# Optimization experiments

Hardware: AMD Instinct MI355X
Metric: run time of the kernel (lower is better)

## Reference

```python
import jax, jax.numpy as jnp
import numpy as np

N_NODES = 50000
N_EDGES = 1600000
IN_CH = 128
HID = 32
HEADS = 2
OUT_CH = 128
N_GRAPHS = 64
NEG_SLOPE = 0.2


def setup_inputs() -> dict:
    key = jax.random.key(0)
    ks = jax.random.split(key, 12)
    x = jax.random.normal(ks[0], (N_NODES, IN_CH), dtype=jnp.float32)
    edge_index = jax.random.randint(ks[1], (2, N_EDGES), 0, N_NODES, dtype=jnp.int64)
    batch = jnp.sort(jax.random.randint(ks[2], (N_NODES,), 0, N_GRAPHS, dtype=jnp.int64))
    s = 0.1
    return {
        "x": x,
        "edge_index": edge_index,
        "batch": batch,
        # conv1: GATConv(IN_CH, 32, heads=2), concat=True -> out 64
        "W1": jax.random.normal(ks[3], (IN_CH, HEADS * HID), dtype=jnp.float32) * s,
        "att_src1": jax.random.normal(ks[4], (HEADS, HID), dtype=jnp.float32) * s,
        "att_dst1": jax.random.normal(ks[5], (HEADS, HID), dtype=jnp.float32) * s,
        "b1": jnp.zeros((HEADS * HID,), dtype=jnp.float32),
        # conv2: GATConv(64, OUT_CH, heads=1)
        "W2": jax.random.normal(ks[6], (HEADS * HID, OUT_CH), dtype=jnp.float32) * s,
        "att_src2": jax.random.normal(ks[7], (1, OUT_CH), dtype=jnp.float32) * s,
        "att_dst2": jax.random.normal(ks[8], (1, OUT_CH), dtype=jnp.float32) * s,
        "b2": jnp.zeros((OUT_CH,), dtype=jnp.float32),
    }


def gat_conv(x, src, dst, W, att_src, att_dst, bias, heads, out_dim):
    """PyG GATConv: edges src->dst, softmax over incoming edges per dst node."""
    n = x.shape[0]
    xl = (x @ W).reshape(n, heads, out_dim)                 # [N,H,D]
    a_s = jnp.sum(xl * att_src, axis=-1)                    # [N,H]
    a_d = jnp.sum(xl * att_dst, axis=-1)                    # [N,H]
    e = jax.nn.leaky_relu(a_s[src] + a_d[dst], NEG_SLOPE)   # [E,H]
    e_max = jax.lax.stop_gradient(jax.ops.segment_max(e, dst, num_segments=n))
    ex = jnp.exp(e - e_max[dst])
    denom = jax.ops.segment_sum(ex, dst, num_segments=n)
    alpha = ex / denom[dst]                                 # [E,H]
    msg = xl[src] * alpha[:, :, None]                       # [E,H,D]
    out = jax.ops.segment_sum(msg, dst, num_segments=n)     # [N,H,D]
    return out.reshape(n, heads * out_dim) + bias


def reference(x, edge_index, batch, W1, att_src1, att_dst1, b1, W2, att_src2, att_dst2, b2):
    n = x.shape[0]
    loop = jnp.arange(n, dtype=edge_index.dtype)
    src = jnp.concatenate([edge_index[0], loop])  # add_self_loops (PyG default)
    dst = jnp.concatenate([edge_index[1], loop])
    h = gat_conv(x, src, dst, W1, att_src1, att_dst1, b1, HEADS, HID)
    h = jax.nn.elu(h)
    h = gat_conv(h, src, dst, W2, att_src2, att_dst2, b2, 1, OUT_CH)
    h = jax.nn.elu(h)
    # global_mean_pool
    sums = jax.ops.segment_sum(h, batch, num_segments=N_GRAPHS)
    cnts = jax.ops.segment_sum(jnp.ones((n,), dtype=h.dtype), batch, num_segments=N_GRAPHS)
    return sums / jnp.maximum(cnts, 1.0)[:, None]
```

## Files before the change

### kernel.cpp

```cpp
#include <hip/hip_runtime.h>

#define N_NODES 50000
#define N_EDGES 1600000
#define E_TOT   (N_EDGES + N_NODES)
#define IN_CH   128
#define C1      64
#define OUT_CH  128
#define N_GRAPHS 64
#define NEG_SLOPE 0.2f

#define BSH   7
#define NBUCK ((N_NODES + 127) / 128)
#define BCAP  5120
#define CHUNK 8192
#define PN    32

typedef __attribute__((ext_vector_type(8))) short bf16x8;
typedef __attribute__((ext_vector_type(4))) float f32x4;

__device__ __forceinline__ float elu_f(float v) {
    return v > 0.f ? v : (__expf(v) - 1.f);
}
__device__ __forceinline__ unsigned short f2bf(float f) {
    unsigned u = __float_as_uint(f);
    return (unsigned short)((u + 0x7FFFu + ((u >> 16) & 1u)) >> 16);
}
__device__ __forceinline__ float bf_lo(unsigned u) { return __uint_as_float(u << 16); }
__device__ __forceinline__ float bf_hi(unsigned u) { return __uint_as_float(u & 0xFFFF0000u); }

__global__ __launch_bounds__(256) void k_gemm1(
    const float* __restrict__ x, const float* __restrict__ W1,
    const float* __restrict__ att_s, const float* __restrict__ att_d,
    unsigned short* __restrict__ xl1, float* __restrict__ a_s, float* __restrict__ a_d)
{
    __shared__ unsigned short W1T[64][136];
    __shared__ float psA[4][16], psD[4][16];
    const int t = threadIdx.x, wave = t >> 6, lane = t & 63;
    const int quad = lane >> 4, lm = lane & 15;
    for (int i = t; i < 128 * 64; i += 256)
        W1T[i & 63][i >> 6] = f2bf(W1[i]);
    __syncthreads();

    const int n0 = wave * 16;
    const int c  = n0 + lm;
    bf16x8 bfr[4];
    #pragma unroll
    for (int s = 0; s < 4; ++s)
        bfr[s] = *(const bf16x8*)&W1T[c][s * 32 + quad * 8];
    const float asc = att_s[c], adc = att_d[c];

    const int r0 = blockIdx.x * 16;
    f32x4 acc = {0.f, 0.f, 0.f, 0.f};
    #pragma unroll
    for (int s = 0; s < 4; ++s) {
        const float* xp = &x[(size_t)(r0 + lm) * 128 + s * 32 + quad * 8];
        float4 xa = *(const float4*)xp;
        float4 xb = *(const float4*)(xp + 4);
        bf16x8 afr;
        afr[0] = (short)f2bf(xa.x); afr[1] = (short)f2bf(xa.y);
        afr[2] = (short)f2bf(xa.z); afr[3] = (short)f2bf(xa.w);
        afr[4] = (short)f2bf(xb.x); afr[5] = (short)f2bf(xb.y);
        afr[6] = (short)f2bf(xb.z); afr[7] = (short)f2bf(xb.w);
        acc = __builtin_amdgcn_mfma_f32_16x16x32_bf16(afr, bfr[s], acc, 0, 0, 0);
    }
    float psv[4], pdv[4];
    #pragma unroll
    for (int r = 0; r < 4; ++r) {
        float v = acc[r];
        xl1[(size_t)(r0 + quad * 4 + r) * 64 + c] = f2bf(v);
        psv[r] = v * asc;
        pdv[r] = v * adc;
    }
    #pragma unroll
    for (int ofs = 1; ofs <= 8; ofs <<= 1) {
        #pragma unroll
        for (int r = 0; r < 4; ++r) {
            psv[r] += __shfl_xor(psv[r], ofs, 64);
            pdv[r] += __shfl_xor(pdv[r], ofs, 64);
        }
    }
    if (lm == 0) {
        #pragma unroll
        for (int r = 0; r < 4; ++r) {
            psA[wave][quad * 4 + r] = psv[r];
            psD[wave][quad * 4 + r] = pdv[r];
        }
    }
    __syncthreads();
    if (t < 32) {
        const int row = t & 15, h = t >> 4;
        a_s[(size_t)(r0 + row) * 2 + h] = psA[2 * h][row] + psA[2 * h + 1][row];
        a_d[(size_t)(r0 + row) * 2 + h] = psD[2 * h][row] + psD[2 * h + 1][row];
    }
}

__global__ __launch_bounds__(256) void k_bin(
    const int* __restrict__ ei, int* __restrict__ gcur, unsigned* __restrict__ bbuf)
{
    __shared__ int cnt[512];
    __shared__ int base[NBUCK];
    __shared__ int cnt2[NBUCK];
    __shared__ int gpos[NBUCK];
    __shared__ unsigned stage[CHUNK];
    __shared__ unsigned short bof[CHUNK];
    const int t = threadIdx.x;
    const long long e0 = (long long)blockIdx.x * CHUNK;
    const int nE = (int)min((long long)CHUNK, (long long)E_TOT - e0);

    cnt[t] = 0; cnt[t + 256] = 0;
    for (int b = t; b < NBUCK; b += 256) cnt2[b] = 0;
    __syncthreads();

    const int per = CHUNK / 256;
    int myb[per]; unsigned mye[per];
    #pragma unroll
    for (int i = 0; i < per; ++i) {
        int idx = t + 256 * i;
        myb[i] = -1;
        if (idx < nE) {
            long long e = e0 + idx;
            int s, d;
            if (e < N_EDGES) { s = ei[e]; d = ei[N_EDGES + e]; }
            else             { s = d = (int)(e - N_EDGES); }
            myb[i] = d >> BSH;
            mye[i] = ((unsigned)(d & 127) << 17) | (unsigned)s;
            atomicAdd(&cnt[myb[i]], 1);
        }
    }
    __syncthreads();
    for (int ofs = 1; ofs < 512; ofs <<= 1) {
        int v0 = (t >= ofs) ? cnt[t - ofs] : 0;
        int v1 = cnt[t + 256 - ofs];
        __syncthreads();
        cnt[t] += v0; cnt[t + 256] += v1;
        __syncthreads();
    }
    for (int b = t; b < NBUCK; b += 256) {
        base[b] = (b == 0) ? 0 : cnt[b - 1];
        int c = cnt[b] - base[b];
        gpos[b] = (c > 0) ? atomicAdd(&gcur[b], c) : 0;
    }
    __syncthreads();
    #pragma unroll
    for (int i = 0; i < per; ++i) {
        if (myb[i] >= 0) {
            int slot = base[myb[i]] + atomicAdd(&cnt2[myb[i]], 1);
            stage[slot] = mye[i];
            bof[slot] = (unsigned short)myb[i];
        }
    }
    __syncthreads();
    for (int i = t; i < nE; i += 256) {
        int b = bof[i];
        int pos = gpos[b] + (i - base[b]);
        if (pos < BCAP)
            bbuf[(size_t)b * BCAP + pos] = stage[i];
    }
}

__global__ __launch_bounds__(256) void k_bsort(
    const int* __restrict__ gcur, unsigned* __restrict__ bbuf,
    int* __restrict__ beg, int* __restrict__ end)
{
    __shared__ unsigned est[BCAP];
    __shared__ unsigned sst[BCAP];
    __shared__ int c[128], lbase[128], c2[128];
    const int b = blockIdx.x, t = threadIdx.x;
    const int n = min(gcur[b], BCAP);
    unsigned* reg = bbuf + (size_t)b * BCAP;
    for (int i = t; i < n; i += 256) est[i] = reg[i];
    if (t < 128) { c[t] = 0; c2[t] = 0; }
    __syncthreads();
    for (int i = t; i < n; i += 256) atomicAdd(&c[est[i] >> 17], 1);
    __syncthreads();
    for (int ofs = 1; ofs < 128; ofs <<= 1) {
        int v = (t < 128 && t >= ofs) ? c[t - ofs] : 0;
        __syncthreads();
        if (t < 128) c[t] += v;
        __syncthreads();
    }
    if (t < 128) {
        lbase[t] = (t == 0) ? 0 : c[t - 1];
        int dst = (b << BSH) + t;
        if (dst < N_NODES) {
            beg[dst] = b * BCAP + lbase[t];
            end[dst] = b * BCAP + c[t];
        }
    }
    __syncthreads();
    for (int i = t; i < n; i += 256) {
        unsigned v = est[i];
        int dl = (int)(v >> 17);
        int pos = lbase[dl] + atomicAdd(&c2[dl], 1);
        sst[pos] = v & 0x1FFFFu;
    }
    __syncthreads();
    for (int i = t; i < n; i += 256) reg[i] = sst[i];
}

__global__ __launch_bounds__(256) void k_attn1g2(
    const int* __restrict__ beg_a, const int* __restrict__ end_a,
    const unsigned* __restrict__ csr,
    const float* __restrict__ a_s, const float* __restrict__ a_d,
    const unsigned short* __restrict__ xl,
    const float* __restrict__ b1, const float* __restrict__ W2,
    const float* __restrict__ att_s2, const float* __restrict__ att_d2,
    unsigned* __restrict__ xl2p,
    float* __restrict__ a_s2, float* __restrict__ a_d2)
{
    __shared__ unsigned W2p[C1 * 64];
    __shared__ float hbuf[4][C1];
    const int t = threadIdx.x, wave = t >> 6, lane = t & 63;
    for (int i = t; i < C1 * 64; i += 256) {
        int k = i >> 6, p = i & 63;
        unsigned lo = f2bf(W2[k * 128 + 2 * p]);
        unsigned hi = f2bf(W2[k * 128 + 2 * p + 1]);
        W2p[i] = lo | (hi << 16);
    }
    const int dst = blockIdx.x * 4 + wave;
    const int beg = beg_a[dst], end = end_a[dst];
    const float ad0 = a_d[dst * 2], ad1 = a_d[dst * 2 + 1];
    const int li = lane & 7, sub = lane >> 3;
    const float4 b1a = *(const float4*)&b1[li * 8];
    const float4 b1b = *(const float4*)&b1[li * 8 + 4];
    const float2 as2c = *(const float2*)&att_s2[2 * lane];
    const float2 ad2c = *(const float2*)&att_d2[2 * lane];
    __syncthreads();

    float acc[8];
    #pragma unroll
    for (int i = 0; i < 8; ++i) acc[i] = 0.f;
    float ws0 = 0.f, ws1 = 0.f;
    for (int base = beg; base < end; base += 64) {
        const int cnt = min(64, end - base);
        int s = 0; float w0 = 0.f, w1 = 0.f;
        if (base + lane < end) {
            s = (int)csr[base + lane];
            float e0 = a_s[s * 2] + ad0;     e0 = e0 > 0.f ? e0 : NEG_SLOPE * e0;
            float e1 = a_s[s * 2 + 1] + ad1; e1 = e1 > 0.f ? e1 : NEG_SLOPE * e1;
            w0 = __expf(e0);
            w1 = __expf(e1);
        }
        ws0 += w0; ws1 += w1;
        for (int k = 0; k < cnt; k += 32) {
            {
                const int ia = k + sub;
                int   sa  = __shfl(s, ia, 64);
                float wa0 = __shfl(w0, ia, 64);
                float wa1 = __shfl(w1, ia, 64);
                float wa = (li < 4) ? wa0 : wa1;
                uint4 va = *(const uint4*)&xl[(size_t)sa * 64 + li * 8];
                acc[0] = fmaf(bf_lo(va.x), wa, acc[0]); acc[1] = fmaf(bf_hi(va.x), wa, acc[1]);
                acc[2] = fmaf(bf_lo(va.y), wa, acc[2]); acc[3] = fmaf(bf_hi(va.y), wa, acc[3]);
                acc[4] = fmaf(bf_lo(va.z), wa, acc[4]); acc[5] = fmaf(bf_hi(va.z), wa, acc[5]);
                acc[6] = fmaf(bf_lo(va.w), wa, acc[6]); acc[7] = fmaf(bf_hi(va.w), wa, acc[7]);
            }
            if (k + 8 < cnt) {
                const int ib = k + 8 + sub;
                int   sb  = __shfl(s, ib, 64);
                float wb0 = __shfl(w0, ib, 64);
                float wb1 = __shfl(w1, ib, 64);
                float wb = (li < 4) ? wb0 : wb1;
                uint4 vb = *(const uint4*)&xl[(size_t)sb * 64 + li * 8];
                acc[0] = fmaf(bf_lo(vb.x), wb, acc[0]); acc[1] = fmaf(bf_hi(vb.x), wb, acc[1]);
                acc[2] = fmaf(bf_lo(vb.y), wb, acc[2]); acc[3] = fmaf(bf_hi(vb.y), wb, acc[3]);
                acc[4] = fmaf(bf_lo(vb.z), wb, acc[4]); acc[5] = fmaf(bf_hi(vb.z), wb, acc[5]);
                acc[6] = fmaf(bf_lo(vb.w), wb, acc[6]); acc[7] = fmaf(bf_hi(vb.w), wb, acc[7]);
            }
            if (k + 16 < cnt) {
                const int ic = k + 16 + sub;
                int   sc  = __shfl(s, ic, 64);
                float wc0 = __shfl(w0, ic, 64);
                float wc1 = __shfl(w1, ic, 64);
                float wc = (li < 4) ? wc0 : wc1;
                uint4 vc = *(const uint4*)&xl[(size_t)sc * 64 + li * 8];
                acc[0] = fmaf(bf_lo(vc.x), wc, acc[0]); acc[1] = fmaf(bf_hi(vc.x), wc, acc[1]);
                acc[2] = fmaf(bf_lo(vc.y), wc, acc[2]); acc[3] = fmaf(bf_hi(vc.y), wc, acc[3]);
                acc[4] = fmaf(bf_lo(vc.z), wc, acc[4]); acc[5] = fmaf(bf_hi(vc.z), wc, acc[5]);
                acc[6] = fmaf(bf_lo(vc.w), wc, acc[6]); acc[7] = fmaf(bf_hi(vc.w), wc, acc[7]);
            }
            if (k + 24 < cnt) {
                const int id = k + 24 + sub;
                int   sd  = __shfl(s, id, 64);
                float wd0 = __shfl(w0, id, 64);
                float wd1 = __shfl(w1, id, 64);
                float wd = (li < 4) ? wd0 : wd1;
                uint4 vd = *(const uint4*)&xl[(size_t)sd * 64 + li * 8];
                acc[0] = fmaf(bf_lo(vd.x), wd, acc[0]); acc[1] = fmaf(bf_hi(vd.x), wd, acc[1]);
                acc[2] = fmaf(bf_lo(vd.y), wd, acc[2]); acc[3] = fmaf(bf_hi(vd.y), wd, acc[3]);
                acc[4] = fmaf(bf_lo(vd.z), wd, acc[4]); acc[5] = fmaf(bf_hi(vd.z), wd, acc[5]);
                acc[6] = fmaf(bf_lo(vd.w), wd, acc[6]); acc[7] = fmaf(bf_hi(vd.w), wd, acc[7]);
            }
        }
    }
    #pragma unroll
    for (int ofs = 32; ofs >= 1; ofs >>= 1) {
        ws0 += __shfl_xor(ws0, ofs, 64);
        ws1 += __shfl_xor(ws1, ofs, 64);
    }
    #pragma unroll
    for (int ofs = 8; ofs <= 32; ofs <<= 1) {
        #pragma unroll
        for (int i = 0; i < 8; ++i) acc[i] += __shfl_xor(acc[i], ofs, 64);
    }
    {
        const float inv = 1.f / ((li < 4) ? ws0 : ws1);
        float h0 = elu_f(acc[0] * inv + b1a.x);
        float h1 = elu_f(acc[1] * inv + b1a.y);
        float h2 = elu_f(acc[2] * inv + b1a.z);
        float h3 = elu_f(acc[3] * inv + b1a.w);
        float h4 = elu_f(acc[4] * inv + b1b.x);
        float h5 = elu_f(acc[5] * inv + b1b.y);
        float h6 = elu_f(acc[6] * inv + b1b.z);
        float h7 = elu_f(acc[7] * inv + b1b.w);
        if (sub == 0) {
            float4 p0; p0.x = h0; p0.y = h1; p0.z = h2; p0.w = h3;
            float4 p1; p1.x = h4; p1.y = h5; p1.z = h6; p1.w = h7;
            *(float4*)&hbuf[wave][li * 8]     = p0;
            *(float4*)&hbuf[wave][li * 8 + 4] = p1;
        }
    }
    __syncthreads();

    float o0 = 0.f, o1 = 0.f;
    #pragma unroll
    for (int k = 0; k < C1; k += 2) {
        float2 hk = *(const float2*)&hbuf[wave][k];
        unsigned p0 = W2p[k * 64 + lane];
        unsigned p1 = W2p[(k + 1) * 64 + lane];
        o0 = fmaf(bf_lo(p0), hk.x, o0); o1 = fmaf(bf_hi(p0), hk.x, o1);
        o0 = fmaf(bf_lo(p1), hk.y, o0); o1 = fmaf(bf_hi(p1), hk.y, o1);
    }
    float ps = o0 * as2c.x + o1 * as2c.y;
    float pd = o0 * ad2c.x + o1 * ad2c.y;
    #pragma unroll
    for (int ofs = 32; ofs >= 1; ofs >>= 1) {
        ps += __shfl_xor(ps, ofs, 64);
        pd += __shfl_xor(pd, ofs, 64);
    }
    if (lane == 0) { a_s2[dst] = ps; a_d2[dst] = pd; }
    unsigned pk = (unsigned)f2bf(o0) | ((unsigned)f2bf(o1) << 16);
    xl2p[(size_t)dst * 64 + lane] = pk;
}

__global__ __launch_bounds__(256) void k_attn2(
    const int* __restrict__ beg_a, const int* __restrict__ end_a,
    const unsigned* __restrict__ csr,
    const float* __restrict__ a_s, const float* __restrict__ a_d,
    const unsigned short* __restrict__ xl, float* __restrict__ out)
{
    const int wave = threadIdx.x >> 6, lane = threadIdx.x & 63;
    const int dst = blockIdx.x * 4 + wave;
    const int beg = beg_a[dst], end = end_a[dst];
    const float ad0 = a_d[dst];

    const int li = lane & 15, sub = lane >> 4;
    float acc[8];
    #pragma unroll
    for (int i = 0; i < 8; ++i) acc[i] = 0.f;
    float ws0 = 0.f;
    for (int base = beg; base < end; base += 64) {
        const int cnt = min(64, end - base);
        int s = 0; float w0 = 0.f;
        if (base + lane < end) {
            s = (int)csr[base + lane];
            float e0 = a_s[s] + ad0; e0 = e0 > 0.f ? e0 : NEG_SLOPE * e0;
            w0 = __expf(e0);
        }
        ws0 += w0;
        for (int k = 0; k < cnt; k += 16) {
            {
                const int ia = k + sub;
                int   sa = __shfl(s, ia, 64);
                float wa = __shfl(w0, ia, 64);
                uint4 va = *(const uint4*)&xl[(size_t)sa * 128 + li * 8];
                acc[0] = fmaf(bf_lo(va.x), wa, acc[0]); acc[1] = fmaf(bf_hi(va.x), wa, acc[1]);
                acc[2] = fmaf(bf_lo(va.y), wa, acc[2]); acc[3] = fmaf(bf_hi(va.y), wa, acc[3]);
                acc[4] = fmaf(bf_lo(va.z), wa, acc[4]); acc[5] = fmaf(bf_hi(va.z), wa, acc[5]);
                acc[6] = fmaf(bf_lo(va.w), wa, acc[6]); acc[7] = fmaf(bf_hi(va.w), wa, acc[7]);
            }
            if (k + 4 < cnt) {
                const int ib = k + 4 + sub;
                int   sb = __shfl(s, ib, 64);
                float wb = __shfl(w0, ib, 64);
                uint4 vb = *(const uint4*)&xl[(size_t)sb * 128 + li * 8];
                acc[0] = fmaf(bf_lo(vb.x), wb, acc[0]); acc[1] = fmaf(bf_hi(vb.x), wb, acc[1]);
                acc[2] = fmaf(bf_lo(vb.y), wb, acc[2]); acc[3] = fmaf(bf_hi(vb.y), wb, acc[3]);
                acc[4] = fmaf(bf_lo(vb.z), wb, acc[4]); acc[5] = fmaf(bf_hi(vb.z), wb, acc[5]);
                acc[6] = fmaf(bf_lo(vb.w), wb, acc[6]); acc[7] = fmaf(bf_hi(vb.w), wb, acc[7]);
            }
            if (k + 8 < cnt) {
                const int ic = k + 8 + sub;
                int   sc = __shfl(s, ic, 64);
                float wc = __shfl(w0, ic, 64);
                uint4 vc = *(const uint4*)&xl[(size_t)sc * 128 + li * 8];
                acc[0] = fmaf(bf_lo(vc.x), wc, acc[0]); acc[1] = fmaf(bf_hi(vc.x), wc, acc[1]);
                acc[2] = fmaf(bf_lo(vc.y), wc, acc[2]); acc[3] = fmaf(bf_hi(vc.y), wc, acc[3]);
                acc[4] = fmaf(bf_lo(vc.z), wc, acc[4]); acc[5] = fmaf(bf_hi(vc.z), wc, acc[5]);
                acc[6] = fmaf(bf_lo(vc.w), wc, acc[6]); acc[7] = fmaf(bf_hi(vc.w), wc, acc[7]);
            }
            if (k + 12 < cnt) {
                const int id = k + 12 + sub;
                int   sd = __shfl(s, id, 64);
                float wd = __shfl(w0, id, 64);
                uint4 vd = *(const uint4*)&xl[(size_t)sd * 128 + li * 8];
                acc[0] = fmaf(bf_lo(vd.x), wd, acc[0]); acc[1] = fmaf(bf_hi(vd.x), wd, acc[1]);
                acc[2] = fmaf(bf_lo(vd.y), wd, acc[2]); acc[3] = fmaf(bf_hi(vd.y), wd, acc[3]);
                acc[4] = fmaf(bf_lo(vd.z), wd, acc[4]); acc[5] = fmaf(bf_hi(vd.z), wd, acc[5]);
                acc[6] = fmaf(bf_lo(vd.w), wd, acc[6]); acc[7] = fmaf(bf_hi(vd.w), wd, acc[7]);
            }
        }
    }
    #pragma unroll
    for (int ofs = 32; ofs >= 1; ofs >>= 1)
        ws0 += __shfl_xor(ws0, ofs, 64);
    #pragma unroll
    for (int ofs = 16; ofs <= 32; ofs <<= 1) {
        #pragma unroll
        for (int i = 0; i < 8; ++i) acc[i] += __shfl_xor(acc[i], ofs, 64);
    }
    if (lane < 16) {
        const float inv = 1.f / ws0;
        float4 r0, r1;
        r0.x = acc[0]*inv; r0.y = acc[1]*inv; r0.z = acc[2]*inv; r0.w = acc[3]*inv;
        r1.x = acc[4]*inv; r1.y = acc[5]*inv; r1.z = acc[6]*inv; r1.w = acc[7]*inv;
        *(float4*)&out[(size_t)dst * 128 + li * 8]     = r0;
        *(float4*)&out[(size_t)dst * 128 + li * 8 + 4] = r1;
    }
}

__global__ __launch_bounds__(256) void k_pool(
    const float* __restrict__ out2, const float* __restrict__ b2,
    const int* __restrict__ batch, float* __restrict__ sums, float* __restrict__ cnts)
{
    const int c    = threadIdx.x & 127;
    const int half = threadIdx.x >> 7;
    const int n0   = blockIdx.x * PN;
    const int nb   = n0 + half;
    if (nb >= N_NODES) return;
    const float bc = b2[c];
    float acc = 0.f;
    int cur = batch[nb], cnt = 0;
    for (int i = half; i < PN; i += 2) {
        int n = n0 + i;
        if (n >= N_NODES) break;
        int g = batch[n];
        if (g != cur) {
            atomicAdd(&sums[cur * OUT_CH + c], acc);
            if (c == 0) atomicAdd(&cnts[cur], (float)cnt);
            acc = 0.f; cnt = 0; cur = g;
        }
        acc += elu_f(out2[(size_t)n * OUT_CH + c] + bc);
        cnt++;
    }
    if (cnt > 0) {
        atomicAdd(&sums[cur * OUT_CH + c], acc);
        if (c == 0) atomicAdd(&cnts[cur], (float)cnt);
    }
}

__global__ __launch_bounds__(256) void k_final(
    const float* __restrict__ sums, const float* __restrict__ cnts,
    float* __restrict__ out)
{
    int i = blockIdx.x * 256 + threadIdx.x;
    if (i >= N_GRAPHS * OUT_CH) return;
    out[i] = sums[i] / fmaxf(cnts[i >> 7], 1.f);
}

extern "C" void kernel_launch(void* const* d_in, const int* in_sizes, int n_in,
                              void* d_out, int out_size, void* d_ws, size_t ws_size,
                              hipStream_t stream)
{
    const float* x    = (const float*)d_in[0];
    const int*   ei   = (const int*)d_in[1];
    const int*   batch= (const int*)d_in[2];
    const float* W1   = (const float*)d_in[3];
    const float* as1  = (const float*)d_in[4];
    const float* ad1  = (const float*)d_in[5];
    const float* b1   = (const float*)d_in[6];
    const float* W2   = (const float*)d_in[7];
    const float* as2  = (const float*)d_in[8];
    const float* ad2  = (const float*)d_in[9];
    const float* b2   = (const float*)d_in[10];

    float* ws = (float*)d_ws;
    size_t o = 0;
    unsigned short* xl1b = (unsigned short*)(ws + o); o += (size_t)N_NODES * C1 / 2;
    unsigned*       xl2p = (unsigned*)(ws + o);       o += (size_t)N_NODES * 64;
    float*    a_s1 = ws + o; o += (size_t)N_NODES * 2;
    float*    a_d1 = ws + o; o += (size_t)N_NODES * 2;
    float*    a_s2 = ws + o; o += (size_t)N_NODES;
    float*    a_d2 = ws + o; o += (size_t)N_NODES;
    float*    out2 = ws + o; o += (size_t)N_NODES * OUT_CH;
    unsigned* bbuf = (unsigned*)(ws + o); o += (size_t)NBUCK * BCAP;
    int*      beg  = (int*)(ws + o); o += (size_t)N_NODES;
    int*      end  = (int*)(ws + o); o += (size_t)N_NODES;
    size_t zero_start = o;
    int*      gcur = (int*)(ws + o); o += (size_t)NBUCK;
    float*    sums = ws + o;         o += (size_t)N_GRAPHS * OUT_CH;
    float*    cnts = ws + o;         o += (size_t)N_GRAPHS;
    size_t zero_bytes = (o - zero_start) * sizeof(float);
    hipMemsetAsync(ws + zero_start, 0, zero_bytes, stream);

    const int nchunks = (E_TOT + CHUNK - 1) / CHUNK;
    k_bin<<<nchunks, 256, 0, stream>>>(ei, gcur, bbuf);
    k_bsort<<<NBUCK, 256, 0, stream>>>(gcur, bbuf, beg, end);

    k_gemm1<<<N_NODES / 16, 256, 0, stream>>>(x, W1, as1, ad1, xl1b, a_s1, a_d1);
    k_attn1g2<<<N_NODES / 4, 256, 0, stream>>>(beg, end, bbuf, a_s1, a_d1, xl1b,
                                               b1, W2, as2, ad2, xl2p, a_s2, a_d2);
    k_attn2<<<N_NODES / 4, 256, 0, stream>>>(beg, end, bbuf, a_s2, a_d2,
                                             (const unsigned short*)xl2p, out2);
    k_pool<<<(N_NODES + PN - 1) / PN, 256, 0, stream>>>(out2, b2, batch, sums, cnts);
    k_final<<<(N_GRAPHS * OUT_CH + 255) / 256, 256, 0, stream>>>(sums, cnts, (float*)d_out);
}
```

Baseline: 298.9 us.

## Split layer-2 projection out of attention kernel into separate MFMA GEMM

The second-layer linear projection, previously fused per destination node into the layer-1 attention kernel as scalar FMAs from shared memory, now runs in its own kernel using bf16 MFMA 16x16x32 instructions over 16-row tiles. The layer-1 attention kernel now only writes the ELU-activated hidden features in bf16 to a new buffer. This removes the per-block W2 staging into LDS and the extra __syncthreads from the attention kernel, which may raise its occupancy and cut its instruction count. The cost is an extra kernel launch and a global-memory round trip of the hidden activations, plus an additional bf16 rounding of the hidden features.

New measurement: 282.3 us. -5.6%, faster.

```diff
diff --git a/kernel.cpp b/kernel.cpp
--- a/kernel.cpp
+++ b/kernel.cpp
@@ -198,34 +198,21 @@
     for (int i = t; i < n; i += 256) reg[i] = sst[i];
 }
 
-__global__ __launch_bounds__(256) void k_attn1g2(
+__global__ __launch_bounds__(256) void k_attn1(
     const int* __restrict__ beg_a, const int* __restrict__ end_a,
     const unsigned* __restrict__ csr,
     const float* __restrict__ a_s, const float* __restrict__ a_d,
     const unsigned short* __restrict__ xl,
-    const float* __restrict__ b1, const float* __restrict__ W2,
-    const float* __restrict__ att_s2, const float* __restrict__ att_d2,
-    unsigned* __restrict__ xl2p,
-    float* __restrict__ a_s2, float* __restrict__ a_d2)
-{
-    __shared__ unsigned W2p[C1 * 64];
-    __shared__ float hbuf[4][C1];
-    const int t = threadIdx.x, wave = t >> 6, lane = t & 63;
-    for (int i = t; i < C1 * 64; i += 256) {
-        int k = i >> 6, p = i & 63;
-        unsigned lo = f2bf(W2[k * 128 + 2 * p]);
-        unsigned hi = f2bf(W2[k * 128 + 2 * p + 1]);
-        W2p[i] = lo | (hi << 16);
-    }
+    const float* __restrict__ b1,
+    unsigned short* __restrict__ hout)
+{
+    const int wave = threadIdx.x >> 6, lane = threadIdx.x & 63;
     const int dst = blockIdx.x * 4 + wave;
     const int beg = beg_a[dst], end = end_a[dst];
     const float ad0 = a_d[dst * 2], ad1 = a_d[dst * 2 + 1];
     const int li = lane & 7, sub = lane >> 3;
     const float4 b1a = *(const float4*)&b1[li * 8];
     const float4 b1b = *(const float4*)&b1[li * 8 + 4];
-    const float2 as2c = *(const float2*)&att_s2[2 * lane];
-    const float2 ad2c = *(const float2*)&att_d2[2 * lane];
-    __syncthreads();
 
     float acc[8];
     #pragma unroll
@@ -303,7 +290,7 @@
         #pragma unroll
         for (int i = 0; i < 8; ++i) acc[i] += __shfl_xor(acc[i], ofs, 64);
     }
-    {
+    if (sub == 0) {
         const float inv = 1.f / ((li < 4) ? ws0 : ws1);
         float h0 = elu_f(acc[0] * inv + b1a.x);
         float h1 = elu_f(acc[1] * inv + b1a.y);
@@ -313,34 +300,77 @@
         float h5 = elu_f(acc[5] * inv + b1b.y);
         float h6 = elu_f(acc[6] * inv + b1b.z);
         float h7 = elu_f(acc[7] * inv + b1b.w);
-        if (sub == 0) {
-            float4 p0; p0.x = h0; p0.y = h1; p0.z = h2; p0.w = h3;
-            float4 p1; p1.x = h4; p1.y = h5; p1.z = h6; p1.w = h7;
-            *(float4*)&hbuf[wave][li * 8]     = p0;
-            *(float4*)&hbuf[wave][li * 8 + 4] = p1;
-        }
-    }
-    __syncthreads();
-
-    float o0 = 0.f, o1 = 0.f;
-    #pragma unroll
-    for (int k = 0; k < C1; k += 2) {
-        float2 hk = *(const float2*)&hbuf[wave][k];
-        unsigned p0 = W2p[k * 64 + lane];
-        unsigned p1 = W2p[(k + 1) * 64 + lane];
-        o0 = fmaf(bf_lo(p0), hk.x, o0); o1 = fmaf(bf_hi(p0), hk.x, o1);
-        o0 = fmaf(bf_lo(p1), hk.y, o0); o1 = fmaf(bf_hi(p1), hk.y, o1);
-    }
-    float ps = o0 * as2c.x + o1 * as2c.y;
-    float pd = o0 * ad2c.x + o1 * ad2c.y;
-    #pragma unroll
-    for (int ofs = 32; ofs >= 1; ofs >>= 1) {
-        ps += __shfl_xor(ps, ofs, 64);
-        pd += __shfl_xor(pd, ofs, 64);
-    }
-    if (lane == 0) { a_s2[dst] = ps; a_d2[dst] = pd; }
-    unsigned pk = (unsigned)f2bf(o0) | ((unsigned)f2bf(o1) << 16);
-    xl2p[(size_t)dst * 64 + lane] = pk;
+        uint4 p;
+        p.x = (unsigned)f2bf(h0) | ((unsigned)f2bf(h1) << 16);
+        p.y = (unsigned)f2bf(h2) | ((unsigned)f2bf(h3) << 16);
+        p.z = (unsigned)f2bf(h4) | ((unsigned)f2bf(h5) << 16);
+        p.w = (unsigned)f2bf(h6) | ((unsigned)f2bf(h7) << 16);
+        *(uint4*)&hout[(size_t)dst * 64 + li * 8] = p;
+    }
+}
+
+__global__ __launch_bounds__(256) void k_gemm2m(
+    const unsigned short* __restrict__ h, const float* __restrict__ W2,
+    const float* __restrict__ att_s, const float* __restrict__ att_d,
+    unsigned short* __restrict__ xl2, float* __restrict__ a_s, float* __restrict__ a_d)
+{
+    __shared__ unsigned short W2T[128][72];
+    __shared__ float psA[4][16], psD[4][16];
+    const int t = threadIdx.x, wave = t >> 6, lane = t & 63;
+    const int quad = lane >> 4, lm = lane & 15;
+    for (int i = t; i < 64 * 128; i += 256)
+        W2T[i & 127][i >> 7] = f2bf(W2[i]);
+    __syncthreads();
+
+    const int c0 = wave * 32 + lm;
+    const int c1 = c0 + 16;
+    bf16x8 bfr0[2], bfr1[2];
+    #pragma unroll
+    for (int s = 0; s < 2; ++s) {
+        bfr0[s] = *(const bf16x8*)&W2T[c0][s * 32 + quad * 8];
+        bfr1[s] = *(const bf16x8*)&W2T[c1][s * 32 + quad * 8];
+    }
+    const float as0 = att_s[c0], as1 = att_s[c1];
+    const float ad0 = att_d[c0], ad1 = att_d[c1];
+
+    const int r0 = blockIdx.x * 16;
+    f32x4 acc0 = {0.f, 0.f, 0.f, 0.f}, acc1 = {0.f, 0.f, 0.f, 0.f};
+    #pragma unroll
+    for (int s = 0; s < 2; ++s) {
+        bf16x8 afr = *(const bf16x8*)&h[(size_t)(r0 + lm) * 64 + s * 32 + quad * 8];
+        acc0 = __builtin_amdgcn_mfma_f32_16x16x32_bf16(afr, bfr0[s], acc0, 0, 0, 0);
+        acc1 = __builtin_amdgcn_mfma_f32_16x16x32_bf16(afr, bfr1[s], acc1, 0, 0, 0);
+    }
+    float psv[4], pdv[4];
+    #pragma unroll
+    for (int r = 0; r < 4; ++r) {
+        float v0 = acc0[r], v1 = acc1[r];
+        const size_t row = (size_t)(r0 + quad * 4 + r) * 128;
+        xl2[row + c0] = f2bf(v0);
+        xl2[row + c1] = f2bf(v1);
+        psv[r] = v0 * as0 + v1 * as1;
+        pdv[r] = v0 * ad0 + v1 * ad1;
+    }
+    #pragma unroll
+    for (int ofs = 1; ofs <= 8; ofs <<= 1) {
+        #pragma unroll
+        for (int r = 0; r < 4; ++r) {
+            psv[r] += __shfl_xor(psv[r], ofs, 64);
+            pdv[r] += __shfl_xor(pdv[r], ofs, 64);
+        }
+    }
+    if (lm == 0) {
+        #pragma unroll
+        for (int r = 0; r < 4; ++r) {
+            psA[wave][quad * 4 + r] = psv[r];
+            psD[wave][quad * 4 + r] = pdv[r];
+        }
+    }
+    __syncthreads();
+    if (t < 16) {
+        a_s[r0 + t] = psA[0][t] + psA[1][t] + psA[2][t] + psA[3][t];
+        a_d[r0 + t] = psD[0][t] + psD[1][t] + psD[2][t] + psD[3][t];
+    }
 }
 
 __global__ __launch_bounds__(256) void k_attn2(
@@ -487,7 +517,8 @@
     float* ws = (float*)d_ws;
     size_t o = 0;
     unsigned short* xl1b = (unsigned short*)(ws + o); o += (size_t)N_NODES * C1 / 2;
-    unsigned*       xl2p = (unsigned*)(ws + o);       o += (size_t)N_NODES * 64;
+    unsigned short* hbuf = (unsigned short*)(ws + o); o += (size_t)N_NODES * C1 / 2;
+    unsigned short* xl2b = (unsigned short*)(ws + o); o += (size_t)N_NODES * OUT_CH / 2;
     float*    a_s1 = ws + o; o += (size_t)N_NODES * 2;
     float*    a_d1 = ws + o; o += (size_t)N_NODES * 2;
     float*    a_s2 = ws + o; o += (size_t)N_NODES;
@@ -508,10 +539,9 @@
     k_bsort<<<NBUCK, 256, 0, stream>>>(gcur, bbuf, beg, end);
 
     k_gemm1<<<N_NODES / 16, 256, 0, stream>>>(x, W1, as1, ad1, xl1b, a_s1, a_d1);
-    k_attn1g2<<<N_NODES / 4, 256, 0, stream>>>(beg, end, bbuf, a_s1, a_d1, xl1b,
-                                               b1, W2, as2, ad2, xl2p, a_s2, a_d2);
-    k_attn2<<<N_NODES / 4, 256, 0, stream>>>(beg, end, bbuf, a_s2, a_d2,
-                                             (const unsigned short*)xl2p, out2);
+    k_attn1<<<N_NODES / 4, 256, 0, stream>>>(beg, end, bbuf, a_s1, a_d1, xl1b, b1, hbuf);
+    k_gemm2m<<<(N_NODES + 15) / 16, 256, 0, stream>>>(hbuf, W2, as2, ad2, xl2b, a_s2, a_d2);
+    k_attn2<<<N_NODES / 4, 256, 0, stream>>>(beg, end, bbuf, a_s2, a_d2, xl2b, out2);
     k_pool<<<(N_NODES + PN - 1) / PN, 256, 0, stream>>>(out2, b2, batch, sums, cnts);
     k_final<<<(N_GRAPHS * OUT_CH + 255) / 256, 256, 0, stream>>>(sums, cnts, (float*)d_out);
 }
```
